# Kernel tuning notes

Measured on AMD Instinct MI355X. Metric: run time of the kernel, lower is better.

The kernel has to match this reference:

```python
import jax, jax.numpy as jnp
import numpy as np

INFO = 32  # info_dim


def _resort_perm(new_shape, cluster, old_num_cols):
    # Replicates resort(): column c of resort_mat has its single 1 at row perm[c],
    # so x @ resort_mat == x[..., perm]. (Faithfully reproduces the original
    # old_idx arithmetic, including its old_num_cols choice.)
    n0, n1 = new_shape
    perm = np.zeros(n0 * n1, np.int32)
    counter = 0
    for i in range(n0):
        for j in range(n1):
            filter_idx = (i % cluster[0]) * cluster[0] + (j % cluster[1])
            cluster_idx = (i // cluster[0]) * (n1 // cluster[1]) + (j // cluster[1])
            perm[counter] = filter_idx * old_num_cols + cluster_idx
            counter += 1
    return perm


def setup_inputs() -> dict:
    key = jax.random.key(0)
    ks = iter(jax.random.split(key, 64))
    def w(shape, scale=0.1):
        return jax.random.normal(next(ks), shape, dtype=jnp.float32) * scale
    B = 512
    inp = {"channel": jax.random.normal(next(ks), (B, 10, 16), dtype=jnp.float32)}
    for name, cin in [("l1", 10), ("g1", 10), ("l2", 2 * INFO), ("g2", 2 * INFO),
                      ("l4", 2 * INFO), ("g4", 2 * INFO), ("l5", 2 * INFO), ("g5", 2 * INFO),
                      ("l7", 2 * INFO), ("g7", 2 * INFO)]:
        inp["w_" + name] = w((INFO, cin))
        inp["b_" + name] = w((INFO,))
    for name in ["l3", "g3", "l6", "g6"]:
        inp["w_" + name] = w((9, INFO, 2 * INFO))
        inp["b_" + name] = w((9, INFO))
    inp["w_l8"] = w((1, 2 * INFO))
    inp["b_l8"] = w((1,))
    inp["perm3"] = jnp.asarray(_resort_perm((12, 12), (3, 3), 12))
    inp["perm6"] = jnp.asarray(_resort_perm((36, 36), (3, 3), 108))
    return inp


def _conv1(x, w, b):  # 1x1 Conv1d: [B,C,N] x [O,C] -> [B,O,N]
    return jnp.einsum('bcn,oc->bon', x, w) + b[None, :, None]


def _mean_bcast(x):
    # x @ (ones(N,N)/N) == broadcast mean over width (global_info_... = True)
    return jnp.broadcast_to(x.mean(axis=-1, keepdims=True), x.shape)


def _process_layer(x, wl, bl, wg, bg):
    fl = jax.nn.relu(_conv1(x, wl, bl))
    fg = _mean_bcast(jax.nn.relu(_conv1(x, wg, bg)))
    return jnp.concatenate([fl, fg], axis=1)


def _process_interp(x, wl, bl, wg, bg, perm):
    # wl/wg: [9,O,C]; per-filter [B,2*INFO,N] outputs concatenated along width,
    # then resorted (the one-hot permutation matmul becomes a gather).
    fl = jax.nn.relu(jnp.einsum('bcn,foc->fbon', x, wl) + bl[:, None, :, None])
    fg = _mean_bcast(jax.nn.relu(jnp.einsum('bcn,foc->fbon', x, wg) + bg[:, None, :, None]))
    cat = jnp.concatenate([fl, fg], axis=2)  # [9,B,2*INFO,N]
    f, b, c, n = cat.shape
    wide = jnp.transpose(cat, (1, 2, 0, 3)).reshape(b, c, f * n)  # [B,2*INFO,9N]
    return wide[:, :, perm]


def reference(channel, w_l1, b_l1, w_g1, b_g1, w_l2, b_l2, w_g2, b_g2,
              w_l3, b_l3, w_g3, b_g3, w_l4, b_l4, w_g4, b_g4,
              w_l5, b_l5, w_g5, b_g5, w_l6, b_l6, w_g6, b_g6,
              w_l7, b_l7, w_g7, b_g7, w_l8, b_l8, perm3, perm6):
    f = _process_layer(channel, w_l1, b_l1, w_g1, b_g1)        # [B,64,16]
    f = _process_layer(f, w_l2, b_l2, w_g2, b_g2)              # [B,64,16]
    f = _process_interp(f, w_l3, b_l3, w_g3, b_g3, perm3)      # [B,64,144]
    f = _process_layer(f, w_l4, b_l4, w_g4, b_g4)              # [B,64,144]
    f = _process_layer(f, w_l5, b_l5, w_g5, b_g5)              # [B,64,144]
    f = _process_interp(f, w_l6, b_l6, w_g6, b_g6, perm6)      # [B,64,1296]
    f = _process_layer(f, w_l7, b_l7, w_g7, b_g7)              # [B,64,1296]
    return _conv1(f, w_l8, b_l8) * np.pi                       # [B,1,1296]
```

## Files before the change

### kernel.cpp

```cpp
#include <hip/hip_runtime.h>
#include <math.h>

#define PI_F 3.14159265358979323846f
#define XQS 580

__device__ __forceinline__ void conv64_16_lds(
    const float* __restrict__ Ws,
    const float* __restrict__ blv, const float* __restrict__ bgv,
    const float* __restrict__ xin, float* __restrict__ xout,
    int lane, int ob)
{
    int rb = (ob & 3) * 8;
    const float* W  = Ws + ((ob < 4) ? 0 : 2048);
    const float* bv = (ob < 4) ? blv : bgv;
    int crow = (ob < 4) ? rb : 32 + rb;
    int q0 = crow >> 2;

    int colA = lane, colB = lane + 64, colC = 128 + (lane & 15);
    float accA[8], accB[8], accC[8];
    #pragma unroll
    for (int oi = 0; oi < 8; ++oi) { float bb = bv[rb+oi]; accA[oi] = bb; accB[oi] = bb; accC[oi] = bb; }
    #pragma unroll 4
    for (int c4 = 0; c4 < 16; ++c4) {
        float4 xA = *(const float4*)&xin[c4*XQS + colA*4];
        float4 xB = *(const float4*)&xin[c4*XQS + colB*4];
        float4 xC = *(const float4*)&xin[c4*XQS + colC*4];
        #pragma unroll
        for (int oi = 0; oi < 8; ++oi) {
            float4 w = *(const float4*)&W[(rb+oi)*64 + c4*4];
            accA[oi] = fmaf(w.x, xA.x, accA[oi]); accA[oi] = fmaf(w.y, xA.y, accA[oi]);
            accA[oi] = fmaf(w.z, xA.z, accA[oi]); accA[oi] = fmaf(w.w, xA.w, accA[oi]);
            accB[oi] = fmaf(w.x, xB.x, accB[oi]); accB[oi] = fmaf(w.y, xB.y, accB[oi]);
            accB[oi] = fmaf(w.z, xB.z, accB[oi]); accB[oi] = fmaf(w.w, xB.w, accB[oi]);
            accC[oi] = fmaf(w.x, xC.x, accC[oi]); accC[oi] = fmaf(w.y, xC.y, accC[oi]);
            accC[oi] = fmaf(w.z, xC.z, accC[oi]); accC[oi] = fmaf(w.w, xC.w, accC[oi]);
        }
    }
    *(float4*)&xout[ q0   *XQS + colA*4] = make_float4(fmaxf(accA[0],0.f),fmaxf(accA[1],0.f),fmaxf(accA[2],0.f),fmaxf(accA[3],0.f));
    *(float4*)&xout[(q0+1)*XQS + colA*4] = make_float4(fmaxf(accA[4],0.f),fmaxf(accA[5],0.f),fmaxf(accA[6],0.f),fmaxf(accA[7],0.f));
    *(float4*)&xout[ q0   *XQS + colB*4] = make_float4(fmaxf(accB[0],0.f),fmaxf(accB[1],0.f),fmaxf(accB[2],0.f),fmaxf(accB[3],0.f));
    *(float4*)&xout[(q0+1)*XQS + colB*4] = make_float4(fmaxf(accB[4],0.f),fmaxf(accB[5],0.f),fmaxf(accB[6],0.f),fmaxf(accB[7],0.f));
    if (lane < 16) {
        *(float4*)&xout[ q0   *XQS + colC*4] = make_float4(fmaxf(accC[0],0.f),fmaxf(accC[1],0.f),fmaxf(accC[2],0.f),fmaxf(accC[3],0.f));
        *(float4*)&xout[(q0+1)*XQS + colC*4] = make_float4(fmaxf(accC[4],0.f),fmaxf(accC[5],0.f),fmaxf(accC[6],0.f),fmaxf(accC[7],0.f));
    }
}

__device__ __forceinline__ void gmean_fill(float* __restrict__ xout, float* __restrict__ gmp,
                                           float* __restrict__ xms, int tid)
{
    __syncthreads();
    if (tid < 128) {
        int j = tid >> 2, q = tid & 3;
        int cc = 32 + j; int qr = cc >> 2, cb = cc & 3;
        float s = 0.f;
        for (int col = q*36; col < q*36+36; ++col) s += xout[qr*XQS + col*4 + cb];
        gmp[tid] = s;
    }
    __syncthreads();
    if (tid < 32) xms[tid] = (gmp[tid*4]+gmp[tid*4+1]+gmp[tid*4+2]+gmp[tid*4+3]) * (1.f/144.f);
    __syncthreads();
    for (int t = tid; t < 4608; t += 512) {
        int col = t >> 5, j = t & 31;
        int cc = 32 + j;
        xout[(cc>>2)*XQS + col*4 + (cc&3)] = xms[j];
    }
    __syncthreads();
}

__global__ __launch_bounds__(512, 2) void kfull(
    const float* __restrict__ ch,
    const float* __restrict__ wl1, const float* __restrict__ bl1,
    const float* __restrict__ wg1, const float* __restrict__ bg1,
    const float* __restrict__ wl2, const float* __restrict__ bl2,
    const float* __restrict__ wg2, const float* __restrict__ bg2,
    const float* __restrict__ wl3, const float* __restrict__ bl3,
    const float* __restrict__ wg3, const float* __restrict__ bg3,
    const float* __restrict__ wl4, const float* __restrict__ bl4,
    const float* __restrict__ wg4, const float* __restrict__ bg4,
    const float* __restrict__ wl5, const float* __restrict__ bl5,
    const float* __restrict__ wg5, const float* __restrict__ bg5,
    const float* __restrict__ wl6, const float* __restrict__ bl6,
    const float* __restrict__ wg6, const float* __restrict__ bg6,
    const float* __restrict__ wl7, const float* __restrict__ bl7,
    const float* __restrict__ wg7, const float* __restrict__ bg7,
    const float* __restrict__ wl8, const float* __restrict__ bl8,
    const int* __restrict__ perm3, const int* __restrict__ perm6,
    float* __restrict__ out)
{
    __shared__ float U[14336];
    __shared__ float xBT[9280];
    __shared__ float W45[8192];
    __shared__ float W7s[2048];
    __shared__ float sgf[448];
    __shared__ float g6m[224];
    __shared__ float bl6s[224];
    __shared__ float wl8s[64];
    __shared__ float xms[32];
    __shared__ float gmp[128];
    __shared__ float l8v[1008];
    __shared__ int   pml[1296];
    __shared__ int   cnt[1008];
    __shared__ int   pfn3[144];
    __shared__ float redbuf[8];
    __shared__ float CbS;

    const int tid = threadIdx.x, lane = tid & 63, wid = tid >> 6;
    const int b = blockIdx.x;
    const int wid_u = __builtin_amdgcn_readfirstlane(wid);

    float* f1s   = U;
    float* gts   = U + 1024;
    float* cat3T = U + 9280;
    float* f2l   = U + 12896;
    float* g3m   = U + 13920;
    float* xls   = U + 14151;
    float* xAT   = U;

    ((float4*)W45)[tid]        = ((const float4*)wl4)[tid];
    ((float4*)W45)[512 + tid]  = ((const float4*)wg4)[tid];
    ((float4*)W45)[1024 + tid] = ((const float4*)wl5)[tid];
    ((float4*)W45)[1536 + tid] = ((const float4*)wg5)[tid];
    {
        int row = tid >> 3, q = tid & 7;
        const float* src = (row < 32) ? (wl7 + row*64) : (wg7 + (row-32)*64);
        *(float4*)&W7s[row*32 + q*4] = *(const float4*)&src[q*4];
    }
    if (tid < 224) bl6s[tid] = bl6[tid];
    if (tid < 64) wl8s[tid] = wl8[tid];
    if (tid < 160) xls[tid] = ch[b*160 + tid];
    if (tid < 144) pfn3[tid] = perm3[tid];
    for (int t = tid; t < 1008; t += 512) cnt[t] = 0;
    __syncthreads();

    for (int t = tid; t < 1296; t += 512) { int p = perm6[t]; pml[t] = p; atomicAdd(&cnt[p], 1); }
    #pragma unroll
    for (int it = 0; it < 2; ++it) {
        int t = tid + it*512; int o = t >> 4, n = t & 15;
        int isg = o >= 32, oo = o & 31;
        const float* w = isg ? wg1 : wl1;
        float acc = (isg ? bg1 : bl1)[oo];
        #pragma unroll
        for (int c = 0; c < 10; ++c) acc = fmaf(w[oo*10+c], xls[c*16+n], acc);
        acc = fmaxf(acc, 0.f);
        if (isg) gts[oo*16+n] = acc; else f1s[o*16+n] = acc;
    }
    __syncthreads();
    if (tid < 32) {
        float s = 0.f;
        #pragma unroll
        for (int n = 0; n < 16; ++n) s += gts[tid*16+n];
        s *= (1.f/16.f);
        #pragma unroll
        for (int n = 0; n < 16; ++n) f1s[(32+tid)*16+n] = s;
    }
    __syncthreads();

    #pragma unroll
    for (int it = 0; it < 2; ++it) {
        int t = tid + it*512; int o = t >> 4, n = t & 15;
        int isg = o >= 32, oo = o & 31;
        const float* w = isg ? wg2 : wl2;
        float acc = (isg ? bg2 : bl2)[oo];
        #pragma unroll
        for (int c = 0; c < 64; ++c) acc = fmaf(w[oo*64+c], f1s[c*16+n], acc);
        acc = fmaxf(acc, 0.f);
        if (isg) gts[oo*16+n] = acc; else f2l[o*16+n] = acc;
    }
    __syncthreads();
    if (tid < 32) {
        float s = 0.f;
        #pragma unroll
        for (int n = 0; n < 16; ++n) s += gts[tid*16+n];
        s *= (1.f/16.f);
        #pragma unroll
        for (int n = 0; n < 16; ++n) f2l[(32+tid)*16+n] = s;
    }
    __syncthreads();

    {
        int n16 = lane & 15, cs = lane >> 4;
        float xr[16];
        #pragma unroll
        for (int i = 0; i < 16; ++i) xr[i] = f2l[cs*256 + i*16 + n16];
        int isg = wid_u >= 4;
        #pragma unroll 2
        for (int k = 0; k < 56; ++k) {
            int r = wid_u*56 + k;
            int rr = isg ? r - 224 : r;
            const float* wrow = (isg ? wg3 : wl3) + rr*64 + cs*16;
            float s0 = 0.f, s1 = 0.f;
            #pragma unroll
            for (int q = 0; q < 4; ++q) {
                float4 w = ((const float4*)wrow)[q];
                if (q & 1) {
                    s1 = fmaf(w.x, xr[q*4+0], s1); s1 = fmaf(w.y, xr[q*4+1], s1);
                    s1 = fmaf(w.z, xr[q*4+2], s1); s1 = fmaf(w.w, xr[q*4+3], s1);
                } else {
                    s0 = fmaf(w.x, xr[q*4+0], s0); s0 = fmaf(w.y, xr[q*4+1], s0);
                    s0 = fmaf(w.z, xr[q*4+2], s0); s0 = fmaf(w.w, xr[q*4+3], s0);
                }
            }
            float s = s0 + s1;
            s += __shfl_xor(s, 16);
            s += __shfl_xor(s, 32);
            s = fmaxf(s + (isg ? bg3 : bl3)[rr], 0.f);
            if (!isg) {
                if (cs == 0) cat3T[n16*226 + rr] = s;
            } else {
                s += __shfl_xor(s, 1); s += __shfl_xor(s, 2);
                s += __shfl_xor(s, 4); s += __shfl_xor(s, 8);
                if (lane == 0) g3m[(rr >> 5)*33 + (rr & 31)] = s * (1.f/16.f);
            }
        }
    }
    __syncthreads();

    for (int t = tid; t < 9216; t += 512) {
        int c4 = t / 576, rem = t - c4*576;
        int col = rem >> 2, ci = rem & 3;
        int c = c4*4 + ci;
        int p3 = pfn3[col]; int pf = p3 >> 4, pn = p3 & 15;
        float v = (c < 32) ? cat3T[pn*226 + pf*32 + c] : g3m[pf*33 + (c - 32)];
        xBT[c4*XQS + col*4 + ci] = v;
    }
    __syncthreads();

    #pragma unroll 1
    for (int L = 0; L < 2; ++L) {
        const float* Ws  = W45 + L*4096;
        const float* blv = L ? bl5 : bl4;
        const float* bgv = L ? bg5 : bg4;
        const float* xin = L ? xAT : xBT;
        float* xout      = L ? xBT : xAT;
        conv64_16_lds(Ws, blv, bgv, xin, xout, lane, wid_u);
        gmean_fill(xout, gmp, xms, tid);
    }

    #pragma unroll
    for (int k = 0; k < 7; ++k) ((float4*)U)[tid + k*512] = ((const float4*)wg6)[tid + k*512];
    __syncthreads();

    {
        int r0 = wid_u*28;
        int c0 = lane, c1 = 64+lane, c2 = 128+(lane&15);
        float4 xc0[8], xc1[8], xc2[8], xmq[8];
        #pragma unroll
        for (int c4 = 0; c4 < 8; ++c4) {
            xc0[c4] = *(const float4*)(xBT + c4*XQS + c0*4);
            xc1[c4] = *(const float4*)(xBT + c4*XQS + c1*4);
            xc2[c4] = *(const float4*)(xBT + c4*XQS + c2*4);
            xmq[c4] = *(const float4*)(xms + c4*4);
        }
        #pragma unroll 1
        for (int k = 0; k < 28; ++k) {
            int r = r0 + k;
            const float* wr = U + r*64;
            float bb = bg6[r];
            #pragma unroll
            for (int c4 = 0; c4 < 8; ++c4) {
                float4 w = *(const float4*)(wr + 32 + c4*4);
                bb = fmaf(w.x, xmq[c4].x, bb); bb = fmaf(w.y, xmq[c4].y, bb);
                bb = fmaf(w.z, xmq[c4].z, bb); bb = fmaf(w.w, xmq[c4].w, bb);
            }
            float a0 = bb, a1 = bb, a2 = bb;
            #pragma unroll
            for (int c4 = 0; c4 < 8; ++c4) {
                float4 w = *(const float4*)(wr + c4*4);
                a0 = fmaf(w.x,xc0[c4].x,a0); a0 = fmaf(w.y,xc0[c4].y,a0); a0 = fmaf(w.z,xc0[c4].z,a0); a0 = fmaf(w.w,xc0[c4].w,a0);
                a1 = fmaf(w.x,xc1[c4].x,a1); a1 = fmaf(w.y,xc1[c4].y,a1); a1 = fmaf(w.z,xc1[c4].z,a1); a1 = fmaf(w.w,xc1[c4].w,a1);
                a2 = fmaf(w.x,xc2[c4].x,a2); a2 = fmaf(w.y,xc2[c4].y,a2); a2 = fmaf(w.z,xc2[c4].z,a2); a2 = fmaf(w.w,xc2[c4].w,a2);
            }
            float s = fmaxf(a0,0.f) + fmaxf(a1,0.f) + ((lane<16) ? fmaxf(a2,0.f) : 0.f);
            s += __shfl_xor(s, 1); s += __shfl_xor(s, 2); s += __shfl_xor(s, 4);
            s += __shfl_xor(s, 8); s += __shfl_xor(s, 16); s += __shfl_xor(s, 32);
            if (lane == 0) g6m[r] = s * (1.f/144.f);
        }
    }
    __syncthreads();

    #pragma unroll
    for (int k = 0; k < 7; ++k) ((float4*)U)[tid + k*512] = ((const float4*)wl6)[tid + k*512];
    if (tid < 448) {
        int f = wid, o7 = lane;
        const float* wr = (o7 < 32) ? (wl7 + o7*64 + 32) : (wg7 + (o7-32)*64 + 32);
        float s = (o7 < 32) ? bl7[o7] : bg7[o7-32];
        #pragma unroll
        for (int i4 = 0; i4 < 8; ++i4) {
            float4 w = ((const float4*)wr)[i4];
            s = fmaf(w.x, g6m[f*32 + i4*4+0], s);
            s = fmaf(w.y, g6m[f*32 + i4*4+1], s);
            s = fmaf(w.z, g6m[f*32 + i4*4+2], s);
            s = fmaf(w.w, g6m[f*32 + i4*4+3], s);
        }
        sgf[f*64 + o7] = s;
    }
    __syncthreads();

    float gacc = 0.f;
    {
        int t = 8*wid_u + (lane >> 3);
        bool valid = t < 63;
        int tt = valid ? t : 62;
        int f = tt / 9;
        int g = tt - f*9;
        int colA = g*16 + (lane & 7);
        int colB = colA + 8;

        float4 xqA[16], xqB[16];
        #pragma unroll
        for (int c4 = 0; c4 < 16; ++c4) {
            xqA[c4] = *(const float4*)(xBT + c4*XQS + colA*4);
            xqB[c4] = *(const float4*)(xBT + c4*XQS + colB*4);
        }
        const float* wf = U + f*2048;
        const float* bf = bl6s + f*32;
        float accA[32], accB[32];
        #pragma unroll
        for (int o = 0; o < 32; ++o) {
            float bb = bf[o];
            float sA = bb, sB = bb;
            const float* w0 = wf + o*64;
            #pragma unroll
            for (int c4 = 0; c4 < 16; ++c4) {
                float4 w = *(const float4*)(w0 + c4*4);
                sA = fmaf(w.x, xqA[c4].x, sA); sA = fmaf(w.y, xqA[c4].y, sA);
                sA = fmaf(w.z, xqA[c4].z, sA); sA = fmaf(w.w, xqA[c4].w, sA);
                sB = fmaf(w.x, xqB[c4].x, sB); sB = fmaf(w.y, xqB[c4].y, sB);
                sB = fmaf(w.z, xqB[c4].z, sB); sB = fmaf(w.w, xqB[c4].w, sB);
            }
            accA[o] = fmaxf(sA, 0.f);
            accB[o] = fmaxf(sB, 0.f);
        }
        const float* sgff = sgf + f*64;
        float l8aA = 0.f, l8aB = 0.f, gA = 0.f, gB = 0.f;
        #pragma unroll 1
        for (int o7 = 0; o7 < 32; ++o7) {
            float s0 = sgff[o7];
            float sA = s0, sB = s0;
            const float* wr = W7s + o7*32;
            #pragma unroll
            for (int q = 0; q < 8; ++q) {
                float4 w = *(const float4*)(wr + q*4);
                sA = fmaf(w.x, accA[q*4+0], sA); sA = fmaf(w.y, accA[q*4+1], sA);
                sA = fmaf(w.z, accA[q*4+2], sA); sA = fmaf(w.w, accA[q*4+3], sA);
                sB = fmaf(w.x, accB[q*4+0], sB); sB = fmaf(w.y, accB[q*4+1], sB);
                sB = fmaf(w.z, accB[q*4+2], sB); sB = fmaf(w.w, accB[q*4+3], sB);
            }
            float wgt = wl8s[o7];
            l8aA = fmaf(wgt, fmaxf(sA, 0.f), l8aA);
            l8aB = fmaf(wgt, fmaxf(sB, 0.f), l8aB);
        }
        #pragma unroll 1
        for (int o7 = 0; o7 < 32; ++o7) {
            float s0 = sgff[32+o7];
            float sA = s0, sB = s0;
            const float* wr = W7s + (32+o7)*32;
            #pragma unroll
            for (int q = 0; q < 8; ++q) {
                float4 w = *(const float4*)(wr + q*4);
                sA = fmaf(w.x, accA[q*4+0], sA); sA = fmaf(w.y, accA[q*4+1], sA);
                sA = fmaf(w.z, accA[q*4+2], sA); sA = fmaf(w.w, accA[q*4+3], sA);
                sB = fmaf(w.x, accB[q*4+0], sB); sB = fmaf(w.y, accB[q*4+1], sB);
                sB = fmaf(w.z, accB[q*4+2], sB); sB = fmaf(w.w, accB[q*4+3], sB);
            }
            float wgt = wl8s[32+o7];
            gA = fmaf(wgt, fmaxf(sA, 0.f), gA);
            gB = fmaf(wgt, fmaxf(sB, 0.f), gB);
        }
        if (valid) {
            l8v[f*144 + colA] = l8aA;
            l8v[f*144 + colB] = l8aB;
            gacc = fmaf((float)cnt[f*144 + colA], gA, gacc);
            gacc = fmaf((float)cnt[f*144 + colB], gB, gacc);
        }
    }

    #pragma unroll
    for (int off = 32; off > 0; off >>= 1) gacc += __shfl_down(gacc, off);
    if (lane == 0) redbuf[wid] = gacc;
    __syncthreads();
    if (tid == 0) {
        float s = 0.f;
        #pragma unroll
        for (int i = 0; i < 8; ++i) s += redbuf[i];
        CbS = bl8[0] + s * (1.f/1296.f);
    }
    __syncthreads();
    float Cb = CbS;
    for (int t = tid; t < 1296; t += 512)
        out[b*1296 + t] = PI_F * (l8v[pml[t]] + Cb);
}

extern "C" void kernel_launch(void* const* d_in, const int* in_sizes, int n_in,
                              void* d_out, int out_size, void* d_ws, size_t ws_size,
                              hipStream_t stream) {
    (void)in_sizes; (void)n_in; (void)out_size; (void)d_ws; (void)ws_size;
    const float* ch  = (const float*)d_in[0];
    const float* wl1 = (const float*)d_in[1];  const float* bl1v = (const float*)d_in[2];
    const float* wg1 = (const float*)d_in[3];  const float* bg1v = (const float*)d_in[4];
    const float* wl2 = (const float*)d_in[5];  const float* bl2v = (const float*)d_in[6];
    const float* wg2 = (const float*)d_in[7];  const float* bg2v = (const float*)d_in[8];
    const float* wl4 = (const float*)d_in[9];  const float* bl4v = (const float*)d_in[10];
    const float* wg4 = (const float*)d_in[11]; const float* bg4v = (const float*)d_in[12];
    const float* wl5 = (const float*)d_in[13]; const float* bl5v = (const float*)d_in[14];
    const float* wg5 = (const float*)d_in[15]; const float* bg5v = (const float*)d_in[16];
    const float* wl7 = (const float*)d_in[17]; const float* bl7v = (const float*)d_in[18];
    const float* wg7 = (const float*)d_in[19]; const float* bg7v = (const float*)d_in[20];
    const float* wl3 = (const float*)d_in[21]; const float* bl3v = (const float*)d_in[22];
    const float* wg3 = (const float*)d_in[23]; const float* bg3v = (const float*)d_in[24];
    const float* wl6 = (const float*)d_in[25]; const float* bl6v = (const float*)d_in[26];
    const float* wg6 = (const float*)d_in[27]; const float* bg6v = (const float*)d_in[28];
    const float* wl8 = (const float*)d_in[29]; const float* bl8v = (const float*)d_in[30];
    const int* perm3 = (const int*)d_in[31];
    const int* perm6 = (const int*)d_in[32];
    float* out = (float*)d_out;

    kfull<<<512, 512, 0, stream>>>(ch,
        wl1, bl1v, wg1, bg1v, wl2, bl2v, wg2, bg2v,
        wl3, bl3v, wg3, bg3v, wl4, bl4v, wg4, bg4v,
        wl5, bl5v, wg5, bg5v, wl6, bl6v, wg6, bg6v,
        wl7, bl7v, wg7, bg7v, wl8, bl8v, perm3, perm6, out);
}
```

Measured before the change: 313.6 us.

## Process two batch samples per block and fold global-mean terms into biases

```diff
diff --git a/kernel.cpp b/kernel.cpp
--- a/kernel.cpp
+++ b/kernel.cpp
@@ -3,69 +3,104 @@
 
 #define PI_F 3.14159265358979323846f
 #define XQS 580
-
-__device__ __forceinline__ void conv64_16_lds(
-    const float* __restrict__ Ws,
-    const float* __restrict__ blv, const float* __restrict__ bgv,
-    const float* __restrict__ xin, float* __restrict__ xout,
-    int lane, int ob)
+#define XB_B 4640
+
+__device__ __forceinline__ void conv32K(
+    const float* __restrict__ Wh,
+    const float* __restrict__ xin,
+    float* __restrict__ xout,
+    const float* __restrict__ m0, const float* __restrict__ m1, const float* __restrict__ m2,
+    const float* __restrict__ m3, const float* __restrict__ m4, const float* __restrict__ m5,
+    float* __restrict__ xmsOut, int lane, int wid_u)
 {
-    int rb = (ob & 3) * 8;
-    const float* W  = Ws + ((ob < 4) ? 0 : 2048);
-    const float* bv = (ob < 4) ? blv : bgv;
-    int crow = (ob < 4) ? rb : 32 + rb;
-    int q0 = crow >> 2;
-
-    int colA = lane, colB = lane + 64, colC = 128 + (lane & 15);
-    float accA[8], accB[8], accC[8];
+    int isg = wid_u >= 4, rb = (wid_u & 3) * 8;
+    int rowbase = isg * 32 + rb;
+    int cA = lane, cB = 64 + lane, cC = 128 + (lane & 15);
+    float a0[8], a1[8], a2[8], a3[8], a4[8], a5[8];
     #pragma unroll
-    for (int oi = 0; oi < 8; ++oi) { float bb = bv[rb+oi]; accA[oi] = bb; accB[oi] = bb; accC[oi] = bb; }
-    #pragma unroll 4
-    for (int c4 = 0; c4 < 16; ++c4) {
-        float4 xA = *(const float4*)&xin[c4*XQS + colA*4];
-        float4 xB = *(const float4*)&xin[c4*XQS + colB*4];
-        float4 xC = *(const float4*)&xin[c4*XQS + colC*4];
+    for (int i = 0; i < 8; ++i) { a0[i]=0.f;a1[i]=0.f;a2[i]=0.f;a3[i]=0.f;a4[i]=0.f;a5[i]=0.f; }
+    #pragma unroll 1
+    for (int kb = 0; kb < 4; ++kb) {
+        int ca = kb*2, cb = kb*2 + 1;
+        float4 xA0 = *(const float4*)&xin[ca*XQS + cA*4];
+        float4 xA1 = *(const float4*)&xin[cb*XQS + cA*4];
+        float4 xB0 = *(const float4*)&xin[ca*XQS + cB*4];
+        float4 xB1 = *(const float4*)&xin[cb*XQS + cB*4];
+        float4 xC0 = *(const float4*)&xin[ca*XQS + cC*4];
+        float4 xC1 = *(const float4*)&xin[cb*XQS + cC*4];
+        float4 yA0 = *(const float4*)&xin[XB_B + ca*XQS + cA*4];
+        float4 yA1 = *(const float4*)&xin[XB_B + cb*XQS + cA*4];
+        float4 yB0 = *(const float4*)&xin[XB_B + ca*XQS + cB*4];
+        float4 yB1 = *(const float4*)&xin[XB_B + cb*XQS + cB*4];
+        float4 yC0 = *(const float4*)&xin[XB_B + ca*XQS + cC*4];
+        float4 yC1 = *(const float4*)&xin[XB_B + cb*XQS + cC*4];
+        const float* wb = Wh + rowbase*32 + kb*8;
         #pragma unroll
         for (int oi = 0; oi < 8; ++oi) {
-            float4 w = *(const float4*)&W[(rb+oi)*64 + c4*4];
-            accA[oi] = fmaf(w.x, xA.x, accA[oi]); accA[oi] = fmaf(w.y, xA.y, accA[oi]);
-            accA[oi] = fmaf(w.z, xA.z, accA[oi]); accA[oi] = fmaf(w.w, xA.w, accA[oi]);
-            accB[oi] = fmaf(w.x, xB.x, accB[oi]); accB[oi] = fmaf(w.y, xB.y, accB[oi]);
-            accB[oi] = fmaf(w.z, xB.z, accB[oi]); accB[oi] = fmaf(w.w, xB.w, accB[oi]);
-            accC[oi] = fmaf(w.x, xC.x, accC[oi]); accC[oi] = fmaf(w.y, xC.y, accC[oi]);
-            accC[oi] = fmaf(w.z, xC.z, accC[oi]); accC[oi] = fmaf(w.w, xC.w, accC[oi]);
-        }
-    }
-    *(float4*)&xout[ q0   *XQS + colA*4] = make_float4(fmaxf(accA[0],0.f),fmaxf(accA[1],0.f),fmaxf(accA[2],0.f),fmaxf(accA[3],0.f));
-    *(float4*)&xout[(q0+1)*XQS + colA*4] = make_float4(fmaxf(accA[4],0.f),fmaxf(accA[5],0.f),fmaxf(accA[6],0.f),fmaxf(accA[7],0.f));
-    *(float4*)&xout[ q0   *XQS + colB*4] = make_float4(fmaxf(accB[0],0.f),fmaxf(accB[1],0.f),fmaxf(accB[2],0.f),fmaxf(accB[3],0.f));
-    *(float4*)&xout[(q0+1)*XQS + colB*4] = make_float4(fmaxf(accB[4],0.f),fmaxf(accB[5],0.f),fmaxf(accB[6],0.f),fmaxf(accB[7],0.f));
-    if (lane < 16) {
-        *(float4*)&xout[ q0   *XQS + colC*4] = make_float4(fmaxf(accC[0],0.f),fmaxf(accC[1],0.f),fmaxf(accC[2],0.f),fmaxf(accC[3],0.f));
-        *(float4*)&xout[(q0+1)*XQS + colC*4] = make_float4(fmaxf(accC[4],0.f),fmaxf(accC[5],0.f),fmaxf(accC[6],0.f),fmaxf(accC[7],0.f));
-    }
-}
-
-__device__ __forceinline__ void gmean_fill(float* __restrict__ xout, float* __restrict__ gmp,
-                                           float* __restrict__ xms, int tid)
-{
-    __syncthreads();
-    if (tid < 128) {
-        int j = tid >> 2, q = tid & 3;
-        int cc = 32 + j; int qr = cc >> 2, cb = cc & 3;
-        float s = 0.f;
-        for (int col = q*36; col < q*36+36; ++col) s += xout[qr*XQS + col*4 + cb];
-        gmp[tid] = s;
-    }
-    __syncthreads();
-    if (tid < 32) xms[tid] = (gmp[tid*4]+gmp[tid*4+1]+gmp[tid*4+2]+gmp[tid*4+3]) * (1.f/144.f);
-    __syncthreads();
-    for (int t = tid; t < 4608; t += 512) {
-        int col = t >> 5, j = t & 31;
-        int cc = 32 + j;
-        xout[(cc>>2)*XQS + col*4 + (cc&3)] = xms[j];
-    }
-    __syncthreads();
+            float4 w0 = *(const float4*)&wb[oi*32];
+            float4 w1 = *(const float4*)&wb[oi*32 + 4];
+            a0[oi] = fmaf(w0.x,xA0.x,a0[oi]); a0[oi] = fmaf(w0.y,xA0.y,a0[oi]);
+            a0[oi] = fmaf(w0.z,xA0.z,a0[oi]); a0[oi] = fmaf(w0.w,xA0.w,a0[oi]);
+            a0[oi] = fmaf(w1.x,xA1.x,a0[oi]); a0[oi] = fmaf(w1.y,xA1.y,a0[oi]);
+            a0[oi] = fmaf(w1.z,xA1.z,a0[oi]); a0[oi] = fmaf(w1.w,xA1.w,a0[oi]);
+            a1[oi] = fmaf(w0.x,xB0.x,a1[oi]); a1[oi] = fmaf(w0.y,xB0.y,a1[oi]);
+            a1[oi] = fmaf(w0.z,xB0.z,a1[oi]); a1[oi] = fmaf(w0.w,xB0.w,a1[oi]);
+            a1[oi] = fmaf(w1.x,xB1.x,a1[oi]); a1[oi] = fmaf(w1.y,xB1.y,a1[oi]);
+            a1[oi] = fmaf(w1.z,xB1.z,a1[oi]); a1[oi] = fmaf(w1.w,xB1.w,a1[oi]);
+            a2[oi] = fmaf(w0.x,xC0.x,a2[oi]); a2[oi] = fmaf(w0.y,xC0.y,a2[oi]);
+            a2[oi] = fmaf(w0.z,xC0.z,a2[oi]); a2[oi] = fmaf(w0.w,xC0.w,a2[oi]);
+            a2[oi] = fmaf(w1.x,xC1.x,a2[oi]); a2[oi] = fmaf(w1.y,xC1.y,a2[oi]);
+            a2[oi] = fmaf(w1.z,xC1.z,a2[oi]); a2[oi] = fmaf(w1.w,xC1.w,a2[oi]);
+            a3[oi] = fmaf(w0.x,yA0.x,a3[oi]); a3[oi] = fmaf(w0.y,yA0.y,a3[oi]);
+            a3[oi] = fmaf(w0.z,yA0.z,a3[oi]); a3[oi] = fmaf(w0.w,yA0.w,a3[oi]);
+            a3[oi] = fmaf(w1.x,yA1.x,a3[oi]); a3[oi] = fmaf(w1.y,yA1.y,a3[oi]);
+            a3[oi] = fmaf(w1.z,yA1.z,a3[oi]); a3[oi] = fmaf(w1.w,yA1.w,a3[oi]);
+            a4[oi] = fmaf(w0.x,yB0.x,a4[oi]); a4[oi] = fmaf(w0.y,yB0.y,a4[oi]);
+            a4[oi] = fmaf(w0.z,yB0.z,a4[oi]); a4[oi] = fmaf(w0.w,yB0.w,a4[oi]);
+            a4[oi] = fmaf(w1.x,yB1.x,a4[oi]); a4[oi] = fmaf(w1.y,yB1.y,a4[oi]);
+            a4[oi] = fmaf(w1.z,yB1.z,a4[oi]); a4[oi] = fmaf(w1.w,yB1.w,a4[oi]);
+            a5[oi] = fmaf(w0.x,yC0.x,a5[oi]); a5[oi] = fmaf(w0.y,yC0.y,a5[oi]);
+            a5[oi] = fmaf(w0.z,yC0.z,a5[oi]); a5[oi] = fmaf(w0.w,yC0.w,a5[oi]);
+            a5[oi] = fmaf(w1.x,yC1.x,a5[oi]); a5[oi] = fmaf(w1.y,yC1.y,a5[oi]);
+            a5[oi] = fmaf(w1.z,yC1.z,a5[oi]); a5[oi] = fmaf(w1.w,yC1.w,a5[oi]);
+        }
+    }
+    #pragma unroll
+    for (int oi = 0; oi < 8; ++oi) {
+        int row = rowbase + oi;
+        a0[oi] = fmaxf(a0[oi] + m0[row], 0.f);
+        a1[oi] = fmaxf(a1[oi] + m1[row], 0.f);
+        a2[oi] = fmaxf(a2[oi] + m2[row], 0.f);
+        a3[oi] = fmaxf(a3[oi] + m3[row], 0.f);
+        a4[oi] = fmaxf(a4[oi] + m4[row], 0.f);
+        a5[oi] = fmaxf(a5[oi] + m5[row], 0.f);
+    }
+    if (!isg) {
+        int q0 = rb >> 2;
+        *(float4*)&xout[ q0   *XQS + cA*4] = make_float4(a0[0],a0[1],a0[2],a0[3]);
+        *(float4*)&xout[(q0+1)*XQS + cA*4] = make_float4(a0[4],a0[5],a0[6],a0[7]);
+        *(float4*)&xout[ q0   *XQS + cB*4] = make_float4(a1[0],a1[1],a1[2],a1[3]);
+        *(float4*)&xout[(q0+1)*XQS + cB*4] = make_float4(a1[4],a1[5],a1[6],a1[7]);
+        *(float4*)&xout[XB_B +  q0   *XQS + cA*4] = make_float4(a3[0],a3[1],a3[2],a3[3]);
+        *(float4*)&xout[XB_B + (q0+1)*XQS + cA*4] = make_float4(a3[4],a3[5],a3[6],a3[7]);
+        *(float4*)&xout[XB_B +  q0   *XQS + cB*4] = make_float4(a4[0],a4[1],a4[2],a4[3]);
+        *(float4*)&xout[XB_B + (q0+1)*XQS + cB*4] = make_float4(a4[4],a4[5],a4[6],a4[7]);
+        if (lane < 16) {
+            *(float4*)&xout[ q0   *XQS + cC*4] = make_float4(a2[0],a2[1],a2[2],a2[3]);
+            *(float4*)&xout[(q0+1)*XQS + cC*4] = make_float4(a2[4],a2[5],a2[6],a2[7]);
+            *(float4*)&xout[XB_B +  q0   *XQS + cC*4] = make_float4(a5[0],a5[1],a5[2],a5[3]);
+            *(float4*)&xout[XB_B + (q0+1)*XQS + cC*4] = make_float4(a5[4],a5[5],a5[6],a5[7]);
+        }
+    } else {
+        #pragma unroll
+        for (int oi = 0; oi < 8; ++oi) {
+            float s0 = a0[oi] + a1[oi] + ((lane < 16) ? a2[oi] : 0.f);
+            float s1 = a3[oi] + a4[oi] + ((lane < 16) ? a5[oi] : 0.f);
+            #pragma unroll
+            for (int off = 1; off < 64; off <<= 1) { s0 += __shfl_xor(s0, off); s1 += __shfl_xor(s1, off); }
+            if (lane == 0) { xmsOut[rb + oi] = s0 * (1.f/144.f); xmsOut[32 + rb + oi] = s1 * (1.f/144.f); }
+        }
+    }
 }
 
 __global__ __launch_bounds__(512, 2) void kfull(
@@ -89,307 +124,407 @@
     float* __restrict__ out)
 {
     __shared__ float U[14336];
-    __shared__ float xBT[9280];
-    __shared__ float W45[8192];
+    __shared__ float xB[9280];
+    __shared__ float W45h[4096];
     __shared__ float W7s[2048];
-    __shared__ float sgf[448];
-    __shared__ float g6m[224];
-    __shared__ float bl6s[224];
+    __shared__ float mp4[896];
+    __shared__ float mp5[128];
+    __shared__ float mp6[448];
+    __shared__ float mpg6[448];
+    __shared__ float sgf[896];
+    __shared__ float g6m[448];
     __shared__ float wl8s[64];
-    __shared__ float xms[32];
-    __shared__ float gmp[128];
-    __shared__ float l8v[1008];
+    __shared__ float xms4[64];
+    __shared__ float xms5[64];
+    __shared__ float l8v[2016];
     __shared__ int   pml[1296];
     __shared__ int   cnt[1008];
     __shared__ int   pfn3[144];
-    __shared__ float redbuf[8];
-    __shared__ float CbS;
+    __shared__ float redbuf[16];
+    __shared__ float CbS[2];
 
     const int tid = threadIdx.x, lane = tid & 63, wid = tid >> 6;
-    const int b = blockIdx.x;
+    const int blk = blockIdx.x;
     const int wid_u = __builtin_amdgcn_readfirstlane(wid);
 
     float* f1s   = U;
-    float* gts   = U + 1024;
-    float* cat3T = U + 9280;
-    float* f2l   = U + 12896;
-    float* g3m   = U + 13920;
-    float* xls   = U + 14151;
-    float* xAT   = U;
-
-    ((float4*)W45)[tid]        = ((const float4*)wl4)[tid];
-    ((float4*)W45)[512 + tid]  = ((const float4*)wg4)[tid];
-    ((float4*)W45)[1024 + tid] = ((const float4*)wl5)[tid];
-    ((float4*)W45)[1536 + tid] = ((const float4*)wg5)[tid];
+    float* gts   = U + 2048;
+    float* f2l   = U + 3072;
+    float* cat3T = U + 5120;
+    float* g3m   = U + 12352;
+    float* xls   = U + 12814;
+    float* x4s   = U;
+    float* wg6h  = U;
+    float* wl6h  = U + 7168;
+
+    for (int t = tid; t < 1024; t += 512) {
+        int l = t >> 9, rem = t & 511;
+        int row = rem >> 3, q = rem & 7;
+        const float* src = l ? ((row < 32) ? wl5 + row*64 : wg5 + (row-32)*64)
+                             : ((row < 32) ? wl4 + row*64 : wg4 + (row-32)*64);
+        *(float4*)&W45h[l*2048 + row*32 + q*4] = *(const float4*)&src[q*4];
+    }
     {
         int row = tid >> 3, q = tid & 7;
         const float* src = (row < 32) ? (wl7 + row*64) : (wg7 + (row-32)*64);
         *(float4*)&W7s[row*32 + q*4] = *(const float4*)&src[q*4];
     }
-    if (tid < 224) bl6s[tid] = bl6[tid];
     if (tid < 64) wl8s[tid] = wl8[tid];
-    if (tid < 160) xls[tid] = ch[b*160 + tid];
+    if (tid < 320) { int b = tid >= 160, i = tid - b*160; xls[b*160 + i] = ch[(2*blk + b)*160 + i]; }
     if (tid < 144) pfn3[tid] = perm3[tid];
     for (int t = tid; t < 1008; t += 512) cnt[t] = 0;
     __syncthreads();
 
     for (int t = tid; t < 1296; t += 512) { int p = perm6[t]; pml[t] = p; atomicAdd(&cnt[p], 1); }
     #pragma unroll
-    for (int it = 0; it < 2; ++it) {
-        int t = tid + it*512; int o = t >> 4, n = t & 15;
+    for (int it = 0; it < 4; ++it) {
+        int t = tid + it*512; int b = t >> 10, o = (t >> 4) & 63, n = t & 15;
         int isg = o >= 32, oo = o & 31;
         const float* w = isg ? wg1 : wl1;
         float acc = (isg ? bg1 : bl1)[oo];
         #pragma unroll
-        for (int c = 0; c < 10; ++c) acc = fmaf(w[oo*10+c], xls[c*16+n], acc);
+        for (int c = 0; c < 10; ++c) acc = fmaf(w[oo*10+c], xls[b*160 + c*16+n], acc);
         acc = fmaxf(acc, 0.f);
-        if (isg) gts[oo*16+n] = acc; else f1s[o*16+n] = acc;
-    }
-    __syncthreads();
-    if (tid < 32) {
+        if (isg) gts[b*512 + oo*16+n] = acc; else f1s[b*1024 + o*16+n] = acc;
+    }
+    __syncthreads();
+    if (tid < 64) {
+        int b = tid >> 5, j = tid & 31;
         float s = 0.f;
         #pragma unroll
-        for (int n = 0; n < 16; ++n) s += gts[tid*16+n];
+        for (int n = 0; n < 16; ++n) s += gts[b*512 + j*16+n];
         s *= (1.f/16.f);
         #pragma unroll
-        for (int n = 0; n < 16; ++n) f1s[(32+tid)*16+n] = s;
+        for (int n = 0; n < 16; ++n) f1s[b*1024 + (32+j)*16+n] = s;
     }
     __syncthreads();
 
     #pragma unroll
-    for (int it = 0; it < 2; ++it) {
-        int t = tid + it*512; int o = t >> 4, n = t & 15;
+    for (int it = 0; it < 4; ++it) {
+        int t = tid + it*512; int b = t >> 10, o = (t >> 4) & 63, n = t & 15;
         int isg = o >= 32, oo = o & 31;
         const float* w = isg ? wg2 : wl2;
         float acc = (isg ? bg2 : bl2)[oo];
         #pragma unroll
-        for (int c = 0; c < 64; ++c) acc = fmaf(w[oo*64+c], f1s[c*16+n], acc);
+        for (int c = 0; c < 64; ++c) acc = fmaf(w[oo*64+c], f1s[b*1024 + c*16+n], acc);
         acc = fmaxf(acc, 0.f);
-        if (isg) gts[oo*16+n] = acc; else f2l[o*16+n] = acc;
-    }
-    __syncthreads();
-    if (tid < 32) {
+        if (isg) gts[b*512 + oo*16+n] = acc; else f2l[b*1024 + o*16+n] = acc;
+    }
+    __syncthreads();
+    if (tid < 64) {
+        int b = tid >> 5, j = tid & 31;
         float s = 0.f;
         #pragma unroll
-        for (int n = 0; n < 16; ++n) s += gts[tid*16+n];
+        for (int n = 0; n < 16; ++n) s += gts[b*512 + j*16+n];
         s *= (1.f/16.f);
         #pragma unroll
-        for (int n = 0; n < 16; ++n) f2l[(32+tid)*16+n] = s;
+        for (int n = 0; n < 16; ++n) f2l[b*1024 + (32+j)*16+n] = s;
     }
     __syncthreads();
 
     {
         int n16 = lane & 15, cs = lane >> 4;
-        float xr[16];
-        #pragma unroll
-        for (int i = 0; i < 16; ++i) xr[i] = f2l[cs*256 + i*16 + n16];
+        float xr0[16], xr1[16];
+        #pragma unroll
+        for (int i = 0; i < 16; ++i) {
+            xr0[i] = f2l[cs*256 + i*16 + n16];
+            xr1[i] = f2l[1024 + cs*256 + i*16 + n16];
+        }
         int isg = wid_u >= 4;
         #pragma unroll 2
         for (int k = 0; k < 56; ++k) {
             int r = wid_u*56 + k;
             int rr = isg ? r - 224 : r;
             const float* wrow = (isg ? wg3 : wl3) + rr*64 + cs*16;
-            float s0 = 0.f, s1 = 0.f;
+            float p0 = 0.f, p1 = 0.f;
             #pragma unroll
             for (int q = 0; q < 4; ++q) {
                 float4 w = ((const float4*)wrow)[q];
-                if (q & 1) {
-                    s1 = fmaf(w.x, xr[q*4+0], s1); s1 = fmaf(w.y, xr[q*4+1], s1);
-                    s1 = fmaf(w.z, xr[q*4+2], s1); s1 = fmaf(w.w, xr[q*4+3], s1);
-                } else {
-                    s0 = fmaf(w.x, xr[q*4+0], s0); s0 = fmaf(w.y, xr[q*4+1], s0);
-                    s0 = fmaf(w.z, xr[q*4+2], s0); s0 = fmaf(w.w, xr[q*4+3], s0);
+                p0 = fmaf(w.x, xr0[q*4+0], p0); p0 = fmaf(w.y, xr0[q*4+1], p0);
+                p0 = fmaf(w.z, xr0[q*4+2], p0); p0 = fmaf(w.w, xr0[q*4+3], p0);
+                p1 = fmaf(w.x, xr1[q*4+0], p1); p1 = fmaf(w.y, xr1[q*4+1], p1);
+                p1 = fmaf(w.z, xr1[q*4+2], p1); p1 = fmaf(w.w, xr1[q*4+3], p1);
+            }
+            p0 += __shfl_xor(p0, 16); p0 += __shfl_xor(p0, 32);
+            p1 += __shfl_xor(p1, 16); p1 += __shfl_xor(p1, 32);
+            float bb = (isg ? bg3 : bl3)[rr];
+            p0 = fmaxf(p0 + bb, 0.f); p1 = fmaxf(p1 + bb, 0.f);
+            if (!isg) {
+                if (cs == 0) { cat3T[n16*226 + rr] = p0; cat3T[3616 + n16*226 + rr] = p1; }
+            } else {
+                p0 += __shfl_xor(p0, 1); p0 += __shfl_xor(p0, 2);
+                p0 += __shfl_xor(p0, 4); p0 += __shfl_xor(p0, 8);
+                p1 += __shfl_xor(p1, 1); p1 += __shfl_xor(p1, 2);
+                p1 += __shfl_xor(p1, 4); p1 += __shfl_xor(p1, 8);
+                if (lane == 0) {
+                    g3m[(rr >> 5)*33 + (rr & 31)] = p0 * (1.f/16.f);
+                    g3m[231 + (rr >> 5)*33 + (rr & 31)] = p1 * (1.f/16.f);
                 }
             }
-            float s = s0 + s1;
-            s += __shfl_xor(s, 16);
-            s += __shfl_xor(s, 32);
-            s = fmaxf(s + (isg ? bg3 : bl3)[rr], 0.f);
-            if (!isg) {
-                if (cs == 0) cat3T[n16*226 + rr] = s;
-            } else {
-                s += __shfl_xor(s, 1); s += __shfl_xor(s, 2);
-                s += __shfl_xor(s, 4); s += __shfl_xor(s, 8);
-                if (lane == 0) g3m[(rr >> 5)*33 + (rr & 31)] = s * (1.f/16.f);
+        }
+    }
+    __syncthreads();
+
+    for (int t = tid; t < 9216; t += 512) {
+        int b = t / 4608, rem = t - b*4608;
+        int c4 = rem / 576, r2 = rem - c4*576;
+        int col = r2 >> 2, ci = r2 & 3, c = c4*4 + ci;
+        int p3 = pfn3[col]; int pf = p3 >> 4, pn = p3 & 15;
+        xB[b*XB_B + c4*XQS + col*4 + ci] = cat3T[b*3616 + pn*226 + pf*32 + c];
+    }
+    for (int t = tid; t < 896; t += 512) {
+        int b = t >= 448, t2 = t - b*448;
+        int pf = t2 >> 6, row = t2 & 63;
+        const float* w = ((row < 32) ? wl4 + row*64 : wg4 + (row-32)*64) + 32;
+        float s = (row < 32) ? bl4[row] : bg4[row-32];
+        #pragma unroll
+        for (int q = 0; q < 8; ++q) {
+            float4 wv = ((const float4*)w)[q];
+            s = fmaf(wv.x, g3m[b*231 + pf*33 + q*4+0], s);
+            s = fmaf(wv.y, g3m[b*231 + pf*33 + q*4+1], s);
+            s = fmaf(wv.z, g3m[b*231 + pf*33 + q*4+2], s);
+            s = fmaf(wv.w, g3m[b*231 + pf*33 + q*4+3], s);
+        }
+        mp4[b*448 + pf*64 + row] = s;
+    }
+    __syncthreads();
+
+    {
+        int pA = pfn3[lane] >> 4;
+        int pB = pfn3[64 + lane] >> 4;
+        int pC = pfn3[128 + (lane & 15)] >> 4;
+        conv32K(W45h, xB, x4s,
+                mp4 + pA*64, mp4 + pB*64, mp4 + pC*64,
+                mp4 + 448 + pA*64, mp4 + 448 + pB*64, mp4 + 448 + pC*64,
+                xms4, lane, wid_u);
+    }
+    __syncthreads();
+    if (tid < 128) {
+        int b = tid >= 64, row = tid & 63;
+        const float* w = ((row < 32) ? wl5 + row*64 : wg5 + (row-32)*64) + 32;
+        float s = (row < 32) ? bl5[row] : bg5[row-32];
+        #pragma unroll
+        for (int q = 0; q < 8; ++q) {
+            float4 wv = ((const float4*)w)[q];
+            s = fmaf(wv.x, xms4[b*32 + q*4+0], s);
+            s = fmaf(wv.y, xms4[b*32 + q*4+1], s);
+            s = fmaf(wv.z, xms4[b*32 + q*4+2], s);
+            s = fmaf(wv.w, xms4[b*32 + q*4+3], s);
+        }
+        mp5[tid] = s;
+    }
+    __syncthreads();
+    conv32K(W45h + 2048, x4s, xB,
+            mp5, mp5, mp5, mp5 + 64, mp5 + 64, mp5 + 64,
+            xms5, lane, wid_u);
+    __syncthreads();
+
+    #pragma unroll
+    for (int k = 0; k < 7; ++k) {
+        int t = tid + k*512;
+        int half = t >= 1792, t2 = t - half*1792;
+        int row = t2 >> 3, q = t2 & 7;
+        const float* src = half ? (wl6 + row*64) : (wg6 + row*64);
+        *(float4*)&U[half*7168 + row*32 + q*4] = *(const float4*)&src[q*4];
+    }
+    for (int t = tid; t < 896; t += 512) {
+        int b = t >= 448, t2 = t - b*448;
+        int isw = t2 >= 224, row = t2 - isw*224;
+        const float* w = (isw ? wl6 + row*64 : wg6 + row*64) + 32;
+        float s = isw ? bl6[row] : bg6[row];
+        #pragma unroll
+        for (int q = 0; q < 8; ++q) {
+            float4 wv = ((const float4*)w)[q];
+            s = fmaf(wv.x, xms5[b*32 + q*4+0], s);
+            s = fmaf(wv.y, xms5[b*32 + q*4+1], s);
+            s = fmaf(wv.z, xms5[b*32 + q*4+2], s);
+            s = fmaf(wv.w, xms5[b*32 + q*4+3], s);
+        }
+        if (isw) mp6[b*224 + row] = s; else mpg6[b*224 + row] = s;
+    }
+    __syncthreads();
+
+    {
+        int bb = wid_u >= 4, w4 = wid_u & 3;
+        int r0 = w4 * 56;
+        int c0 = lane, c1 = 64 + lane, c2 = 128 + (lane & 15);
+        const float* xb = xB + bb*XB_B;
+        float4 xc0[8], xc1[8], xc2[8];
+        #pragma unroll
+        for (int q = 0; q < 8; ++q) {
+            xc0[q] = *(const float4*)&xb[q*XQS + c0*4];
+            xc1[q] = *(const float4*)&xb[q*XQS + c1*4];
+            xc2[q] = *(const float4*)&xb[q*XQS + c2*4];
+        }
+        #pragma unroll 1
+        for (int k = 0; k < 56; ++k) {
+            int r = r0 + k;
+            const float* wr = wg6h + r*32;
+            float bb0 = mpg6[bb*224 + r];
+            float v0 = bb0, v1 = bb0, v2 = bb0;
+            #pragma unroll
+            for (int q = 0; q < 8; ++q) {
+                float4 w = *(const float4*)&wr[q*4];
+                v0 = fmaf(w.x,xc0[q].x,v0); v0 = fmaf(w.y,xc0[q].y,v0); v0 = fmaf(w.z,xc0[q].z,v0); v0 = fmaf(w.w,xc0[q].w,v0);
+                v1 = fmaf(w.x,xc1[q].x,v1); v1 = fmaf(w.y,xc1[q].y,v1); v1 = fmaf(w.z,xc1[q].z,v1); v1 = fmaf(w.w,xc1[q].w,v1);
+                v2 = fmaf(w.x,xc2[q].x,v2); v2 = fmaf(w.y,xc2[q].y,v2); v2 = fmaf(w.z,xc2[q].z,v2); v2 = fmaf(w.w,xc2[q].w,v2);
             }
-        }
-    }
-    __syncthreads();
-
-    for (int t = tid; t < 9216; t += 512) {
-        int c4 = t / 576, rem = t - c4*576;
-        int col = rem >> 2, ci = rem & 3;
-        int c = c4*4 + ci;
-        int p3 = pfn3[col]; int pf = p3 >> 4, pn = p3 & 15;
-        float v = (c < 32) ? cat3T[pn*226 + pf*32 + c] : g3m[pf*33 + (c - 32)];
-        xBT[c4*XQS + col*4 + ci] = v;
-    }
-    __syncthreads();
-
-    #pragma unroll 1
-    for (int L = 0; L < 2; ++L) {
-        const float* Ws  = W45 + L*4096;
-        const float* blv = L ? bl5 : bl4;
-        const float* bgv = L ? bg5 : bg4;
-        const float* xin = L ? xAT : xBT;
-        float* xout      = L ? xBT : xAT;
-        conv64_16_lds(Ws, blv, bgv, xin, xout, lane, wid_u);
-        gmean_fill(xout, gmp, xms, tid);
-    }
-
-    #pragma unroll
-    for (int k = 0; k < 7; ++k) ((float4*)U)[tid + k*512] = ((const float4*)wg6)[tid + k*512];
-    __syncthreads();
-
-    {
-        int r0 = wid_u*28;
-        int c0 = lane, c1 = 64+lane, c2 = 128+(lane&15);
-        float4 xc0[8], xc1[8], xc2[8], xmq[8];
-        #pragma unroll
-        for (int c4 = 0; c4 < 8; ++c4) {
-            xc0[c4] = *(const float4*)(xBT + c4*XQS + c0*4);
-            xc1[c4] = *(const float4*)(xBT + c4*XQS + c1*4);
-            xc2[c4] = *(const float4*)(xBT + c4*XQS + c2*4);
-            xmq[c4] = *(const float4*)(xms + c4*4);
-        }
-        #pragma unroll 1
-        for (int k = 0; k < 28; ++k) {
-            int r = r0 + k;
-            const float* wr = U + r*64;
-            float bb = bg6[r];
-            #pragma unroll
-            for (int c4 = 0; c4 < 8; ++c4) {
-                float4 w = *(const float4*)(wr + 32 + c4*4);
-                bb = fmaf(w.x, xmq[c4].x, bb); bb = fmaf(w.y, xmq[c4].y, bb);
-                bb = fmaf(w.z, xmq[c4].z, bb); bb = fmaf(w.w, xmq[c4].w, bb);
-            }
-            float a0 = bb, a1 = bb, a2 = bb;
-            #pragma unroll
-            for (int c4 = 0; c4 < 8; ++c4) {
-                float4 w = *(const float4*)(wr + c4*4);
-                a0 = fmaf(w.x,xc0[c4].x,a0); a0 = fmaf(w.y,xc0[c4].y,a0); a0 = fmaf(w.z,xc0[c4].z,a0); a0 = fmaf(w.w,xc0[c4].w,a0);
-                a1 = fmaf(w.x,xc1[c4].x,a1); a1 = fmaf(w.y,xc1[c4].y,a1); a1 = fmaf(w.z,xc1[c4].z,a1); a1 = fmaf(w.w,xc1[c4].w,a1);
-                a2 = fmaf(w.x,xc2[c4].x,a2); a2 = fmaf(w.y,xc2[c4].y,a2); a2 = fmaf(w.z,xc2[c4].z,a2); a2 = fmaf(w.w,xc2[c4].w,a2);
-            }
-            float s = fmaxf(a0,0.f) + fmaxf(a1,0.f) + ((lane<16) ? fmaxf(a2,0.f) : 0.f);
-            s += __shfl_xor(s, 1); s += __shfl_xor(s, 2); s += __shfl_xor(s, 4);
-            s += __shfl_xor(s, 8); s += __shfl_xor(s, 16); s += __shfl_xor(s, 32);
-            if (lane == 0) g6m[r] = s * (1.f/144.f);
-        }
-    }
-    __syncthreads();
-
-    #pragma unroll
-    for (int k = 0; k < 7; ++k) ((float4*)U)[tid + k*512] = ((const float4*)wl6)[tid + k*512];
-    if (tid < 448) {
-        int f = wid, o7 = lane;
-        const float* wr = (o7 < 32) ? (wl7 + o7*64 + 32) : (wg7 + (o7-32)*64 + 32);
+            float s = fmaxf(v0,0.f) + fmaxf(v1,0.f) + ((lane < 16) ? fmaxf(v2,0.f) : 0.f);
+            #pragma unroll
+            for (int off = 1; off < 64; off <<= 1) s += __shfl_xor(s, off);
+            if (lane == 0) g6m[bb*224 + r] = s * (1.f/144.f);
+        }
+    }
+    __syncthreads();
+
+    for (int t = tid; t < 896; t += 512) {
+        int b = t >= 448, t2 = t - b*448;
+        int f = t2 >> 6, o7 = t2 & 63;
+        const float* w = ((o7 < 32) ? wl7 + o7*64 : wg7 + (o7-32)*64) + 32;
         float s = (o7 < 32) ? bl7[o7] : bg7[o7-32];
         #pragma unroll
-        for (int i4 = 0; i4 < 8; ++i4) {
-            float4 w = ((const float4*)wr)[i4];
-            s = fmaf(w.x, g6m[f*32 + i4*4+0], s);
-            s = fmaf(w.y, g6m[f*32 + i4*4+1], s);
-            s = fmaf(w.z, g6m[f*32 + i4*4+2], s);
-            s = fmaf(w.w, g6m[f*32 + i4*4+3], s);
-        }
-        sgf[f*64 + o7] = s;
-    }
-    __syncthreads();
-
-    float gacc = 0.f;
+        for (int q = 0; q < 8; ++q) {
+            float4 wv = ((const float4*)w)[q];
+            s = fmaf(wv.x, g6m[b*224 + f*32 + q*4+0], s);
+            s = fmaf(wv.y, g6m[b*224 + f*32 + q*4+1], s);
+            s = fmaf(wv.z, g6m[b*224 + f*32 + q*4+2], s);
+            s = fmaf(wv.w, g6m[b*224 + f*32 + q*4+3], s);
+        }
+        sgf[b*448 + f*64 + o7] = s;
+    }
+    __syncthreads();
+
+    float gacc0 = 0.f, gacc1 = 0.f;
     {
         int t = 8*wid_u + (lane >> 3);
         bool valid = t < 63;
         int tt = valid ? t : 62;
-        int f = tt / 9;
-        int g = tt - f*9;
-        int colA = g*16 + (lane & 7);
-        int colB = colA + 8;
-
-        float4 xqA[16], xqB[16];
-        #pragma unroll
-        for (int c4 = 0; c4 < 16; ++c4) {
-            xqA[c4] = *(const float4*)(xBT + c4*XQS + colA*4);
-            xqB[c4] = *(const float4*)(xBT + c4*XQS + colB*4);
-        }
-        const float* wf = U + f*2048;
-        const float* bf = bl6s + f*32;
-        float accA[32], accB[32];
+        int f = tt / 9, g = tt - f*9;
+        int colA = g*16 + (lane & 7), colB = colA + 8;
+        const float* wfh = wl6h + f*1024;
+
+        float a0A[32], a0B[32], a1A[32], a1B[32];
+        #pragma unroll
+        for (int o = 0; o < 32; ++o) { a0A[o]=0.f; a0B[o]=0.f; a1A[o]=0.f; a1B[o]=0.f; }
+        #pragma unroll 1
+        for (int kb = 0; kb < 4; ++kb) {
+            int ca = kb*2, cb = kb*2 + 1;
+            float4 xA0 = *(const float4*)&xB[ca*XQS + colA*4];
+            float4 xA1 = *(const float4*)&xB[cb*XQS + colA*4];
+            float4 xB0 = *(const float4*)&xB[ca*XQS + colB*4];
+            float4 xB1 = *(const float4*)&xB[cb*XQS + colB*4];
+            float4 yA0 = *(const float4*)&xB[XB_B + ca*XQS + colA*4];
+            float4 yA1 = *(const float4*)&xB[XB_B + cb*XQS + colA*4];
+            float4 yB0 = *(const float4*)&xB[XB_B + ca*XQS + colB*4];
+            float4 yB1 = *(const float4*)&xB[XB_B + cb*XQS + colB*4];
+            const float* wb = wfh + kb*8;
+            #pragma unroll
+            for (int o = 0; o < 32; ++o) {
+                float4 w0 = *(const float4*)&wb[o*32];
+                float4 w1 = *(const float4*)&wb[o*32 + 4];
+                a0A[o] = fmaf(w0.x,xA0.x,a0A[o]); a0A[o] = fmaf(w0.y,xA0.y,a0A[o]);
+                a0A[o] = fmaf(w0.z,xA0.z,a0A[o]); a0A[o] = fmaf(w0.w,xA0.w,a0A[o]);
+                a0A[o] = fmaf(w1.x,xA1.x,a0A[o]); a0A[o] = fmaf(w1.y,xA1.y,a0A[o]);
+                a0A[o] = fmaf(w1.z,xA1.z,a0A[o]); a0A[o] = fmaf(w1.w,xA1.w,a0A[o]);
+                a0B[o] = fmaf(w0.x,xB0.x,a0B[o]); a0B[o] = fmaf(w0.y,xB0.y,a0B[o]);
+                a0B[o] = fmaf(w0.z,xB0.z,a0B[o]); a0B[o] = fmaf(w0.w,xB0.w,a0B[o]);
+                a0B[o] = fmaf(w1.x,xB1.x,a0B[o]); a0B[o] = fmaf(w1.y,xB1.y,a0B[o]);
+                a0B[o] = fmaf(w1.z,xB1.z,a0B[o]); a0B[o] = fmaf(w1.w,xB1.w,a0B[o]);
+                a1A[o] = fmaf(w0.x,yA0.x,a1A[o]); a1A[o] = fmaf(w0.y,yA0.y,a1A[o]);
+                a1A[o] = fmaf(w0.z,yA0.z,a1A[o]); a1A[o] = fmaf(w0.w,yA0.w,a1A[o]);
+                a1A[o] = fmaf(w1.x,yA1.x,a1A[o]); a1A[o] = fmaf(w1.y,yA1.y,a1A[o]);
+                a1A[o] = fmaf(w1.z,yA1.z,a1A[o]); a1A[o] = fmaf(w1.w,yA1.w,a1A[o]);
+                a1B[o] = fmaf(w0.x,yB0.x,a1B[o]); a1B[o] = fmaf(w0.y,yB0.y,a1B[o]);
+                a1B[o] = fmaf(w0.z,yB0.z,a1B[o]); a1B[o] = fmaf(w0.w,yB0.w,a1B[o]);
+                a1B[o] = fmaf(w1.x,yB1.x,a1B[o]); a1B[o] = fmaf(w1.y,yB1.y,a1B[o]);
+                a1B[o] = fmaf(w1.z,yB1.z,a1B[o]); a1B[o] = fmaf(w1.w,yB1.w,a1B[o]);
+            }
+        }
         #pragma unroll
         for (int o = 0; o < 32; ++o) {
-            float bb = bf[o];
-            float sA = bb, sB = bb;
-            const float* w0 = wf + o*64;
-            #pragma unroll
-            for (int c4 = 0; c4 < 16; ++c4) {
-                float4 w = *(const float4*)(w0 + c4*4);
-                sA = fmaf(w.x, xqA[c4].x, sA); sA = fmaf(w.y, xqA[c4].y, sA);
-                sA = fmaf(w.z, xqA[c4].z, sA); sA = fmaf(w.w, xqA[c4].w, sA);
-                sB = fmaf(w.x, xqB[c4].x, sB); sB = fmaf(w.y, xqB[c4].y, sB);
-                sB = fmaf(w.z, xqB[c4].z, sB); sB = fmaf(w.w, xqB[c4].w, sB);
-            }
-            accA[o] = fmaxf(sA, 0.f);
-            accB[o] = fmaxf(sB, 0.f);
-        }
-        const float* sgff = sgf + f*64;
-        float l8aA = 0.f, l8aB = 0.f, gA = 0.f, gB = 0.f;
+            float m0 = mp6[f*32 + o], m1 = mp6[224 + f*32 + o];
+            a0A[o] = fmaxf(a0A[o] + m0, 0.f);
+            a0B[o] = fmaxf(a0B[o] + m0, 0.f);
+            a1A[o] = fmaxf(a1A[o] + m1, 0.f);
+            a1B[o] = fmaxf(a1B[o] + m1, 0.f);
+        }
+        const float* sg0 = sgf + f*64;
+        const float* sg1 = sgf + 448 + f*64;
+        float l80A = 0.f, l80B = 0.f, l81A = 0.f, l81B = 0.f;
+        float g0A = 0.f, g0B = 0.f, g1A = 0.f, g1B = 0.f;
         #pragma unroll 1
         for (int o7 = 0; o7 < 32; ++o7) {
-            float s0 = sgff[o7];
-            float sA = s0, sB = s0;
+            float s0 = sg0[o7], s1 = sg1[o7];
+            float sA0 = s0, sB0 = s0, sA1 = s1, sB1 = s1;
             const float* wr = W7s + o7*32;
             #pragma unroll
             for (int q = 0; q < 8; ++q) {
-                float4 w = *(const float4*)(wr + q*4);
-                sA = fmaf(w.x, accA[q*4+0], sA); sA = fmaf(w.y, accA[q*4+1], sA);
-                sA = fmaf(w.z, accA[q*4+2], sA); sA = fmaf(w.w, accA[q*4+3], sA);
-                sB = fmaf(w.x, accB[q*4+0], sB); sB = fmaf(w.y, accB[q*4+1], sB);
-                sB = fmaf(w.z, accB[q*4+2], sB); sB = fmaf(w.w, accB[q*4+3], sB);
+                float4 w = *(const float4*)&wr[q*4];
+                sA0 = fmaf(w.x,a0A[q*4+0],sA0); sA0 = fmaf(w.y,a0A[q*4+1],sA0);
+                sA0 = fmaf(w.z,a0A[q*4+2],sA0); sA0 = fmaf(w.w,a0A[q*4+3],sA0);
+                sB0 = fmaf(w.x,a0B[q*4+0],sB0); sB0 = fmaf(w.y,a0B[q*4+1],sB0);
+                sB0 = fmaf(w.z,a0B[q*4+2],sB0); sB0 = fmaf(w.w,a0B[q*4+3],sB0);
+                sA1 = fmaf(w.x,a1A[q*4+0],sA1); sA1 = fmaf(w.y,a1A[q*4+1],sA1);
+                sA1 = fmaf(w.z,a1A[q*4+2],sA1); sA1 = fmaf(w.w,a1A[q*4+3],sA1);
+                sB1 = fmaf(w.x,a1B[q*4+0],sB1); sB1 = fmaf(w.y,a1B[q*4+1],sB1);
+                sB1 = fmaf(w.z,a1B[q*4+2],sB1); sB1 = fmaf(w.w,a1B[q*4+3],sB1);
             }
             float wgt = wl8s[o7];
-            l8aA = fmaf(wgt, fmaxf(sA, 0.f), l8aA);
-            l8aB = fmaf(wgt, fmaxf(sB, 0.f), l8aB);
+            l80A = fmaf(wgt, fmaxf(sA0,0.f), l80A);
+            l80B = fmaf(wgt, fmaxf(sB0,0.f), l80B);
+            l81A = fmaf(wgt, fmaxf(sA1,0.f), l81A);
+            l81B = fmaf(wgt, fmaxf(sB1,0.f), l81B);
         }
         #pragma unroll 1
         for (int o7 = 0; o7 < 32; ++o7) {
-            float s0 = sgff[32+o7];
-            float sA = s0, sB = s0;
+            float s0 = sg0[32+o7], s1 = sg1[32+o7];
+            float sA0 = s0, sB0 = s0, sA1 = s1, sB1 = s1;
             const float* wr = W7s + (32+o7)*32;
             #pragma unroll
             for (int q = 0; q < 8; ++q) {
-                float4 w = *(const float4*)(wr + q*4);
-                sA = fmaf(w.x, accA[q*4+0], sA); sA = fmaf(w.y, accA[q*4+1], sA);
-                sA = fmaf(w.z, accA[q*4+2], sA); sA = fmaf(w.w, accA[q*4+3], sA);
-                sB = fmaf(w.x, accB[q*4+0], sB); sB = fmaf(w.y, accB[q*4+1], sB);
-                sB = fmaf(w.z, accB[q*4+2], sB); sB = fmaf(w.w, accB[q*4+3], sB);
+                float4 w = *(const float4*)&wr[q*4];
+                sA0 = fmaf(w.x,a0A[q*4+0],sA0); sA0 = fmaf(w.y,a0A[q*4+1],sA0);
+                sA0 = fmaf(w.z,a0A[q*4+2],sA0); sA0 = fmaf(w.w,a0A[q*4+3],sA0);
+                sB0 = fmaf(w.x,a0B[q*4+0],sB0); sB0 = fmaf(w.y,a0B[q*4+1],sB0);
+                sB0 = fmaf(w.z,a0B[q*4+2],sB0); sB0 = fmaf(w.w,a0B[q*4+3],sB0);
+                sA1 = fmaf(w.x,a1A[q*4+0],sA1); sA1 = fmaf(w.y,a1A[q*4+1],sA1);
+                sA1 = fmaf(w.z,a1A[q*4+2],sA1); sA1 = fmaf(w.w,a1A[q*4+3],sA1);
+                sB1 = fmaf(w.x,a1B[q*4+0],sB1); sB1 = fmaf(w.y,a1B[q*4+1],sB1);
+                sB1 = fmaf(w.z,a1B[q*4+2],sB1); sB1 = fmaf(w.w,a1B[q*4+3],sB1);
             }
             float wgt = wl8s[32+o7];
-            gA = fmaf(wgt, fmaxf(sA, 0.f), gA);
-            gB = fmaf(wgt, fmaxf(sB, 0.f), gB);
+            g0A = fmaf(wgt, fmaxf(sA0,0.f), g0A);
+            g0B = fmaf(wgt, fmaxf(sB0,0.f), g0B);
+            g1A = fmaf(wgt, fmaxf(sA1,0.f), g1A);
+            g1B = fmaf(wgt, fmaxf(sB1,0.f), g1B);
         }
         if (valid) {
-            l8v[f*144 + colA] = l8aA;
-            l8v[f*144 + colB] = l8aB;
-            gacc = fmaf((float)cnt[f*144 + colA], gA, gacc);
-            gacc = fmaf((float)cnt[f*144 + colB], gB, gacc);
+            l8v[f*144 + colA] = l80A;
+            l8v[f*144 + colB] = l80B;
+            l8v[1008 + f*144 + colA] = l81A;
+            l8v[1008 + f*144 + colB] = l81B;
+            gacc0 = fmaf((float)cnt[f*144 + colA], g0A, gacc0);
+            gacc0 = fmaf((float)cnt[f*144 + colB], g0B, gacc0);
+            gacc1 = fmaf((float)cnt[f*144 + colA], g1A, gacc1);
+            gacc1 = fmaf((float)cnt[f*144 + colB], g1B, gacc1);
         }
     }
 
     #pragma unroll
-    for (int off = 32; off > 0; off >>= 1) gacc += __shfl_down(gacc, off);
-    if (lane == 0) redbuf[wid] = gacc;
-    __syncthreads();
-    if (tid == 0) {
+    for (int off = 32; off > 0; off >>= 1) { gacc0 += __shfl_down(gacc0, off); gacc1 += __shfl_down(gacc1, off); }
+    if (lane == 0) { redbuf[wid] = gacc0; redbuf[8 + wid] = gacc1; }
+    __syncthreads();
+    if (tid < 2) {
         float s = 0.f;
         #pragma unroll
-        for (int i = 0; i < 8; ++i) s += redbuf[i];
-        CbS = bl8[0] + s * (1.f/1296.f);
-    }
-    __syncthreads();
-    float Cb = CbS;
-    for (int t = tid; t < 1296; t += 512)
-        out[b*1296 + t] = PI_F * (l8v[pml[t]] + Cb);
+        for (int i = 0; i < 8; ++i) s += redbuf[tid*8 + i];
+        CbS[tid] = bl8[0] + s * (1.f/1296.f);
+    }
+    __syncthreads();
+    for (int t = tid; t < 2592; t += 512) {
+        int b = t >= 1296, idx = t - b*1296;
+        out[(2*blk + b)*1296 + idx] = PI_F * (l8v[b*1008 + pml[idx]] + CbS[b]);
+    }
 }
 
 extern "C" void kernel_launch(void* const* d_in, const int* in_sizes, int n_in,
@@ -416,7 +551,7 @@
     const int* perm6 = (const int*)d_in[32];
     float* out = (float*)d_out;
 
-    kfull<<<512, 512, 0, stream>>>(ch,
+    kfull<<<256, 512, 0, stream>>>(ch,
         wl1, bl1v, wg1, bg1v, wl2, bl2v, wg2, bg2v,
         wl3, bl3v, wg3, bg3v, wl4, bl4v, wg4, bg4v,
         wl5, bl5v, wg5, bg5v, wl6, bl6v, wg6, bg6v,
```

Result: faster. 265.1 us (-15.4%).
